# Optimization experiments

Hardware: AMD Instinct MI355X
Metric: run time of the kernel (lower is better)

The kernel has to match this reference:

```python
import jax, jax.numpy as jnp
import numpy as np

HC = 32  # half_color_channels


def dwconv(x, w, padding):
    # depthwise conv, NCHW / OIHW, groups == channels
    return jax.lax.conv_general_dilated(
        x, w, (1, 1), padding,
        feature_group_count=x.shape[1],
        dimension_numbers=('NCHW', 'OIHW', 'NCHW'))


def setup_inputs() -> dict:
    key = jax.random.key(0)
    ks = jax.random.split(key, 6)
    B, C, H, W = 8, 2 * HC, 256, 256
    mask = jax.random.normal(ks[0], (B, 8, 16, 16), dtype=jnp.float32)  # unused by forward math
    color = jax.random.normal(ks[1], (B, C, H, W), dtype=jnp.float32)
    w_bbx = jax.random.normal(ks[2], (C, 1, 1, 1), dtype=jnp.float32) * 0.2
    w_width = jax.random.normal(ks[3], (HC, 1, 1, 5), dtype=jnp.float32) * 0.2
    w_height = jax.random.normal(ks[4], (HC, 1, 5, 1), dtype=jnp.float32) * 0.2
    w_score = jax.random.normal(ks[5], (1, C, 1, 1), dtype=jnp.float32) * 0.05
    return {"mask": mask, "color": color, "w_bbx": w_bbx,
            "w_width": w_width, "w_height": w_height, "w_score": w_score}


def _forward(color, w_bbx, w_width, w_height, w_score):
    B, C, H, W = color.shape
    # depthwise 1x1 conv == per-channel scale
    wh = color * w_bbx[:, 0, 0, 0][None, :, None, None]
    # even channels -> horizontal (1,5) depthwise, odd -> vertical (5,1) depthwise; max over channels
    wmap = dwconv(wh[:, 0::2], w_width, ((0, 0), (2, 2))).max(axis=1, keepdims=True)
    hmap = dwconv(wh[:, 1::2], w_height, ((2, 2), (0, 0))).max(axis=1, keepdims=True)
    # dense 1x1 conv on the raw input for the score channel
    score = jnp.einsum('bchw,oc->bohw', color, w_score[:, :, 0, 0])
    bbx = jnp.concatenate([score, wmap, hmap], axis=1)  # [B,3,H,W]
    bf = bbx.transpose(0, 2, 3, 1).reshape(B, -1, 3)    # [B,HW,3]
    s = jax.nn.sigmoid(bf[:, :, 0])                      # [B,HW]
    wv = bf[:, :, 0]  # NOTE: faithful to original code, which reuses channel 0 for w
    hv = bf[:, :, 1]  #       and channel 1 for h
    # top-10 per image, then threshold masking
    _, ti = jax.lax.top_k(s, 10)                         # [B,10]
    m = jnp.zeros_like(s, dtype=bool).at[jnp.arange(B)[:, None], ti].set(True)
    m = (m & (s > 0.6)) | (s > 0.8)                      # [B,HW] selection mask
    # coordinate grids in flattened H-major order
    yg = jnp.repeat(jnp.arange(H, dtype=s.dtype), W)[None, :]  # [1,HW]
    xg = jnp.tile(jnp.arange(W, dtype=s.dtype), H)[None, :]
    cw = jnp.exp(wv) * 10.0
    ch = jnp.exp(hv) * 10.0
    x1 = jnp.floor(xg - cw); x2 = jnp.ceil(xg + cw)
    y1 = jnp.floor(yg - ch); y2 = jnp.ceil(yg + ch)
    # clamp out-of-bounds boxes symmetrically around the center
    bad = (x1 < 0) | (x2 > W)
    hw = jnp.minimum(W - xg, xg)
    x1 = jnp.where(bad, jnp.floor(xg - hw), x1)
    x2 = jnp.where(bad, jnp.ceil(xg + hw), x2)
    bad = (y1 < 0) | (y2 > H)
    hh = jnp.minimum(H - yg, yg)
    y1 = jnp.where(bad, jnp.floor(yg - hh), y1)
    y2 = jnp.where(bad, jnp.ceil(yg + hh), y2)
    # dense padded equivalent of boolean compaction: zero out unselected rows
    out = jnp.stack([s, x1, y1, x2, y2], axis=-1) * m[..., None]  # [B,HW,5]
    return score, out, m


def reference(mask, color, w_bbx, w_width, w_height, w_score):
    return _forward(color, w_bbx, w_width, w_height, w_score)
```

## Files before the change

### kernel.cpp

```cpp
#include <hip/hip_runtime.h>
#include <math.h>


__device__ __forceinline__ void insert10(float (&a)[10], float v) {
    if (v > a[9]) {
#pragma unroll
        for (int k = 0; k < 10; ++k) {
            if (v > a[k]) { float t = a[k]; a[k] = v; v = t; }
        }
    }
}

__global__ __launch_bounds__(256, 4) void k_main(
    const float* __restrict__ color,
    const float* __restrict__ w_bbx,
    const float* __restrict__ w_width,
    const float* __restrict__ w_score,
    float* __restrict__ score_out,
    float* __restrict__ wmap_out)
{
    const int tid  = threadIdx.x;
    const int lane = tid & 63;
    const int wid  = tid >> 6;
    const int bid  = blockIdx.x;
    const int b    = bid >> 8;
    const int h    = bid & 255;
    const int w0   = lane << 2;

    const int cg = __builtin_amdgcn_readfirstlane(wid) << 4;

    const float* base = color + ((size_t)b << 22) + ((size_t)h << 8) + (size_t)w0
                              + ((size_t)cg << 16);

    float a0 = 0.f, a1 = 0.f, a2 = 0.f, a3 = 0.f;
    float m0 = -INFINITY, m1 = -INFINITY, m2 = -INFINITY, m3 = -INFINITY;

#pragma unroll
    for (int cc = 0; cc < 16; cc += 2) {
        const float4 v = *reinterpret_cast<const float4*>(base + ((size_t)cc << 16));
        const float4 u = *reinterpret_cast<const float4*>(base + ((size_t)(cc + 1) << 16));
        const int c = cg + cc;
        const float wsc0 = w_score[c];
        const float wsc1 = w_score[c + 1];
        a0 += v.x * wsc0 + u.x * wsc1;
        a1 += v.y * wsc0 + u.y * wsc1;
        a2 += v.z * wsc0 + u.z * wsc1;
        a3 += v.w * wsc0 + u.w * wsc1;

        const float wb = w_bbx[c];
        const float ex = v.x * wb, ey = v.y * wb, ez = v.z * wb, ew = v.w * wb;
        float lm2 = __shfl_up(ez, 1);
        float lm1 = __shfl_up(ew, 1);
        float rp1 = __shfl_down(ex, 1);
        float rp2 = __shfl_down(ey, 1);
        if (lane == 0)  { lm2 = 0.f; lm1 = 0.f; }
        if (lane == 63) { rp1 = 0.f; rp2 = 0.f; }

        const int hc = c >> 1;
        const float t0 = w_width[hc * 5 + 0];
        const float t1 = w_width[hc * 5 + 1];
        const float t2 = w_width[hc * 5 + 2];
        const float t3 = w_width[hc * 5 + 3];
        const float t4 = w_width[hc * 5 + 4];

        m0 = fmaxf(m0, lm2 * t0 + lm1 * t1 + ex * t2 + ey * t3 + ez * t4);
        m1 = fmaxf(m1, lm1 * t0 + ex * t1 + ey * t2 + ez * t3 + ew * t4);
        m2 = fmaxf(m2, ex * t0 + ey * t1 + ez * t2 + ew * t3 + rp1 * t4);
        m3 = fmaxf(m3, ey * t0 + ez * t1 + ew * t2 + rp1 * t3 + rp2 * t4);
    }

    __shared__ float sa[4][256];
    __shared__ float sm[4][256];
    *reinterpret_cast<float4*>(&sa[wid][w0]) = make_float4(a0, a1, a2, a3);
    *reinterpret_cast<float4*>(&sm[wid][w0]) = make_float4(m0, m1, m2, m3);
    __syncthreads();

    const float s = (sa[0][tid] + sa[1][tid]) + (sa[2][tid] + sa[3][tid]);
    const float m = fmaxf(fmaxf(sm[0][tid], sm[1][tid]), fmaxf(sm[2][tid], sm[3][tid]));
    const size_t o = ((size_t)b << 16) + ((size_t)h << 8) + (size_t)tid;
    score_out[o] = s;
    wmap_out[o]  = m;
}

__global__ __launch_bounds__(256) void k_top_a(
    const float* __restrict__ score, float* __restrict__ lists)
{
    const int tid   = threadIdx.x;
    const int slice = blockIdx.x & 7;
    const int b     = blockIdx.x >> 3;
    const float* p  = score + ((size_t)b << 16) + ((size_t)slice << 13);

    float a[10];
#pragma unroll
    for (int k = 0; k < 10; ++k) a[k] = -INFINITY;
    for (int j = tid; j < 8192; j += 256) insert10(a, p[j]);

    __shared__ float buf[256][11];
#pragma unroll
    for (int k = 0; k < 10; ++k) buf[tid][k] = a[k];
    __syncthreads();

    for (int n = 128; n >= 1; n >>= 1) {
        if (tid < n) {
            float bb[10];
#pragma unroll
            for (int k = 0; k < 10; ++k) bb[k] = buf[tid + n][k];
            float c[10];
#pragma unroll
            for (int k = 0; k < 10; ++k) {
                float best = fmaxf(a[k], bb[k]);
#pragma unroll
                for (int i = 0; i < k; ++i) best = fmaxf(best, fminf(a[i], bb[k - 1 - i]));
                c[k] = best;
            }
#pragma unroll
            for (int k = 0; k < 10; ++k) { a[k] = c[k]; buf[tid][k] = c[k]; }
        }
        __syncthreads();
    }
    if (tid == 0) {
#pragma unroll
        for (int k = 0; k < 10; ++k) lists[blockIdx.x * 10 + k] = a[k];
    }
}

__global__ void k_top_b(const float* __restrict__ lists, float* __restrict__ tvals)
{
    const int b = threadIdx.x;
    if (b < 8) {
        float a[10];
#pragma unroll
        for (int k = 0; k < 10; ++k) a[k] = -INFINITY;
        for (int j = 0; j < 80; ++j) insert10(a, lists[b * 80 + j]);
        tvals[b] = a[9];
    }
}

__global__ __launch_bounds__(256) void k_boxes(
    const float* __restrict__ score,
    const float* __restrict__ tvals,
    float* __restrict__ out5,
    float* __restrict__ mout)
{
    const int i   = blockIdx.x * 256 + threadIdx.x;
    const float sc = score[i];
    const float wm = mout[i];
    const int b   = i >> 16;
    const int pix = i & 65535;
    const float tb = tvals[b];

    const double sd  = 1.0 / (1.0 + exp(-(double)sc));
    const bool  top  = (sc >= tb);
    const bool  m    = (top && (sd > 0.6)) || (sd > 0.8);

    const double xg = (double)(pix & 255);
    const double yg = (double)(pix >> 8);
    const double cw = exp((double)sc) * 10.0;
    const double ch = exp((double)wm) * 10.0;

    double x1 = floor(xg - cw), x2 = ceil(xg + cw);
    double y1 = floor(yg - ch), y2 = ceil(yg + ch);
    if ((x1 < 0.0) || (x2 > 256.0)) {
        const double hw = fmin(256.0 - xg, xg);
        x1 = floor(xg - hw); x2 = ceil(xg + hw);
    }
    if ((y1 < 0.0) || (y2 > 256.0)) {
        const double hh = fmin(256.0 - yg, yg);
        y1 = floor(yg - hh); y2 = ceil(yg + hh);
    }

    const float mf = m ? 1.0f : 0.0f;
    const size_t o = (size_t)i * 5;
    out5[o + 0] = mf * (float)sd;
    out5[o + 1] = mf * (float)x1;
    out5[o + 2] = mf * (float)y1;
    out5[o + 3] = mf * (float)x2;
    out5[o + 4] = mf * (float)y2;
    mout[i] = mf;
}

extern "C" void kernel_launch(void* const* d_in, const int* in_sizes, int n_in,
                              void* d_out, int out_size, void* d_ws, size_t ws_size,
                              hipStream_t stream) {
    const float* color   = (const float*)d_in[1];
    const float* w_bbx   = (const float*)d_in[2];
    const float* w_width = (const float*)d_in[3];
    const float* w_score = (const float*)d_in[5];

    float* score_out = (float*)d_out;
    float* out5      = score_out + 524288;
    float* mout      = score_out + 524288 + 2621440;

    float* lists = (float*)d_ws;
    float* tvals = lists + 640;

    k_main <<<2048, 256, 0, stream>>>(color, w_bbx, w_width, w_score, score_out, mout);
    k_top_a<<<64,   256, 0, stream>>>(score_out, lists);
    k_top_b<<<1,    64,  0, stream>>>(lists, tvals);
    k_boxes<<<2048, 256, 0, stream>>>(score_out, tvals, out5, mout);
}
```

Baseline: 237.0 us.

## Fuse per-row top-10 selection into main kernel and collapse top-k stages

Each k_main block now computes a top-10 list of its 256 scores using wave shuffles and a merge network, then writes it to a workspace. A single 8-block reduce kernel merges the 256 per-row lists per image into the threshold. This replaces the separate scan that reread the score map and drops one launch. In exchange, k_main takes on extra shuffle and merge ALU work plus another __syncthreads.

```diff
diff --git a/kernel.cpp b/kernel.cpp
--- a/kernel.cpp
+++ b/kernel.cpp
@@ -1,6 +1,19 @@
 #include <hip/hip_runtime.h>
 #include <math.h>
 
+
+__device__ __forceinline__ void merge10(float (&a)[10], const float (&b)[10]) {
+    float c[10];
+#pragma unroll
+    for (int k = 0; k < 10; ++k) {
+        float best = fmaxf(a[k], b[k]);
+#pragma unroll
+        for (int i = 0; i < k; ++i) best = fmaxf(best, fminf(a[i], b[k - 1 - i]));
+        c[k] = best;
+    }
+#pragma unroll
+    for (int k = 0; k < 10; ++k) a[k] = c[k];
+}
 
 __device__ __forceinline__ void insert10(float (&a)[10], float v) {
     if (v > a[9]) {
@@ -17,7 +30,8 @@
     const float* __restrict__ w_width,
     const float* __restrict__ w_score,
     float* __restrict__ score_out,
-    float* __restrict__ wmap_out)
+    float* __restrict__ wmap_out,
+    float* __restrict__ lists)
 {
     const int tid  = threadIdx.x;
     const int lane = tid & 63;
@@ -80,20 +94,55 @@
     const size_t o = ((size_t)b << 16) + ((size_t)h << 8) + (size_t)tid;
     score_out[o] = s;
     wmap_out[o]  = m;
-}
-
-__global__ __launch_bounds__(256) void k_top_a(
-    const float* __restrict__ score, float* __restrict__ lists)
+
+    float t10[10];
+    t10[0] = s;
+#pragma unroll
+    for (int k = 1; k < 10; ++k) t10[k] = -INFINITY;
+
+#pragma unroll
+    for (int off = 1; off < 64; off <<= 1) {
+        float b10[10];
+#pragma unroll
+        for (int k = 0; k < 10; ++k) b10[k] = __shfl_xor(t10[k], off);
+        merge10(t10, b10);
+    }
+
+    __shared__ float wl[4][10];
+    if (lane == 0) {
+#pragma unroll
+        for (int k = 0; k < 10; ++k) wl[wid][k] = t10[k];
+    }
+    __syncthreads();
+
+    if (tid == 0) {
+        float fa[10], fb[10];
+#pragma unroll
+        for (int k = 0; k < 10; ++k) fa[k] = wl[0][k];
+#pragma unroll
+        for (int k = 0; k < 10; ++k) fb[k] = wl[1][k];
+        merge10(fa, fb);
+#pragma unroll
+        for (int k = 0; k < 10; ++k) fb[k] = wl[2][k];
+        merge10(fa, fb);
+#pragma unroll
+        for (int k = 0; k < 10; ++k) fb[k] = wl[3][k];
+        merge10(fa, fb);
+#pragma unroll
+        for (int k = 0; k < 10; ++k) lists[bid * 10 + k] = fa[k];
+    }
+}
+
+__global__ __launch_bounds__(256) void k_reduce(
+    const float* __restrict__ lists, float* __restrict__ tvals)
 {
-    const int tid   = threadIdx.x;
-    const int slice = blockIdx.x & 7;
-    const int b     = blockIdx.x >> 3;
-    const float* p  = score + ((size_t)b << 16) + ((size_t)slice << 13);
+    const int tid = threadIdx.x;
+    const int b   = blockIdx.x;
+    const float* p = lists + (size_t)b * 2560 + (size_t)tid * 10;
 
     float a[10];
 #pragma unroll
-    for (int k = 0; k < 10; ++k) a[k] = -INFINITY;
-    for (int j = tid; j < 8192; j += 256) insert10(a, p[j]);
+    for (int k = 0; k < 10; ++k) a[k] = p[k];
 
     __shared__ float buf[256][11];
 #pragma unroll
@@ -105,35 +154,13 @@
             float bb[10];
 #pragma unroll
             for (int k = 0; k < 10; ++k) bb[k] = buf[tid + n][k];
-            float c[10];
-#pragma unroll
-            for (int k = 0; k < 10; ++k) {
-                float best = fmaxf(a[k], bb[k]);
-#pragma unroll
-                for (int i = 0; i < k; ++i) best = fmaxf(best, fminf(a[i], bb[k - 1 - i]));
-                c[k] = best;
-            }
-#pragma unroll
-            for (int k = 0; k < 10; ++k) { a[k] = c[k]; buf[tid][k] = c[k]; }
+            merge10(a, bb);
+#pragma unroll
+            for (int k = 0; k < 10; ++k) buf[tid][k] = a[k];
         }
         __syncthreads();
     }
-    if (tid == 0) {
-#pragma unroll
-        for (int k = 0; k < 10; ++k) lists[blockIdx.x * 10 + k] = a[k];
-    }
-}
-
-__global__ void k_top_b(const float* __restrict__ lists, float* __restrict__ tvals)
-{
-    const int b = threadIdx.x;
-    if (b < 8) {
-        float a[10];
-#pragma unroll
-        for (int k = 0; k < 10; ++k) a[k] = -INFINITY;
-        for (int j = 0; j < 80; ++j) insert10(a, lists[b * 80 + j]);
-        tvals[b] = a[9];
-    }
+    if (tid == 0) tvals[b] = a[9];
 }
 
 __global__ __launch_bounds__(256) void k_boxes(
@@ -192,10 +219,9 @@
     float* mout      = score_out + 524288 + 2621440;
 
     float* lists = (float*)d_ws;
-    float* tvals = lists + 640;
-
-    k_main <<<2048, 256, 0, stream>>>(color, w_bbx, w_width, w_score, score_out, mout);
-    k_top_a<<<64,   256, 0, stream>>>(score_out, lists);
-    k_top_b<<<1,    64,  0, stream>>>(lists, tvals);
-    k_boxes<<<2048, 256, 0, stream>>>(score_out, tvals, out5, mout);
-}
+    float* tvals = lists + 20480;
+
+    k_main  <<<2048, 256, 0, stream>>>(color, w_bbx, w_width, w_score, score_out, mout, lists);
+    k_reduce<<<8,    256, 0, stream>>>(lists, tvals);
+    k_boxes <<<2048, 256, 0, stream>>>(score_out, tvals, out5, mout);
+}
```

Measured after the change: 211.7 us. -10.7%, faster.
